# Kernel optimization log

Hardware: AMD Instinct MI355X
Metric: run time of the kernel (lower is better)

Reference implementation:

```python
import jax, jax.numpy as jnp
import numpy as np

N, D = 262144, 64
C, K, NSPLITS = 16, 4 + 12, 4  # K=16 codewords per codebook (2**NSPLITS)
K = 16
M = 16


def setup_inputs() -> dict:
    key = jax.random.key(0)
    k1, k2, k3, k4, k5 = jax.random.split(key, 5)
    A = jax.random.normal(k1, (N, D), dtype=jnp.float32)
    B = jax.random.normal(k2, (M, D), dtype=jnp.float32)
    prototypes = jax.random.normal(k3, (C, K, D), dtype=jnp.float32)
    split_dims = jax.random.randint(k4, (C, NSPLITS), 0, D, dtype=jnp.int32)
    # level i of the binary tree uses 2**i thresholds; pad to 2**(NSPLITS-1)=8
    split_vals = jax.random.normal(k5, (C, NSPLITS, 2 ** (NSPLITS - 1)), dtype=jnp.float32)
    return {"A": A, "B": B, "prototypes": prototypes,
            "split_dims": split_dims, "split_vals": split_vals}


def _encode(A, split_dims, split_vals):
    # Vectorized maddness_encode / apply_hash_function over all C codebooks.
    n = A.shape[0]
    c = split_dims.shape[0]
    nsplits = split_dims.shape[1]
    c_idx = jnp.arange(c)[None, :]                      # [1, C]
    group_ids = jnp.zeros((n, c), dtype=jnp.int32)      # [N, C]
    for i in range(nsplits):                            # fixed tiny loop (4 levels)
        x = A[:, split_dims[:, i]]                      # [N, C] gather of split dim
        vals_i = split_vals[:, i, :]                    # [C, 8]
        v = vals_i[c_idx, group_ids]                    # [N, C] per-group threshold
        group_ids = group_ids * 2 + (x > v).astype(jnp.int32)
    return group_ids                                    # [N, C] in [0, K)


def reference(A, B, prototypes, split_dims, split_vals):
    # 1) encode A rows: binary-tree hash per codebook -> codeword ids
    A_enc = _encode(A, split_dims, split_vals)          # [N, C] int32
    # 2) LUTs: luts[m, c, k] = <B[m], prototypes[c, k]>  (maddness_lut per row)
    luts = jnp.einsum('md,ckd->ckm', B, prototypes)     # [C, K, M]
    # 3) LUT-based accumulate (quantize_lut=False path): sum over codebooks
    c_idx = jnp.arange(luts.shape[0])[None, :]          # [1, C]
    g = luts[c_idx, A_enc]                              # [N, C, M] gathered LUT entries
    out = g.sum(axis=1).T                               # [M, N]
    return out
```

## Files before the change

### kernel.cpp

```cpp
#include <hip/hip_runtime.h>
#include <hip/hip_fp16.h>


#define NROWS 262144
#define DDIM  64
#define TPB   128
#define NBLK  2048
#define RSTR  129
#define LSTR  24

typedef __attribute__((ext_vector_type(8))) _Float16 half8;
typedef __attribute__((ext_vector_type(4))) unsigned int u32x4;

__global__ __launch_bounds__(256) void lut_build(
    const float* __restrict__ B,
    const float* __restrict__ P,
    _Float16* __restrict__ lutw)
{
    int o = blockIdx.x * 256 + threadIdx.x;
    int m  = o & 15;
    int ck = o >> 4;
    const float4* Bp = (const float4*)(B + m * DDIM);
    const float4* Pp = (const float4*)(P + ck * DDIM);
    float dot = 0.f;
    #pragma unroll
    for (int q = 0; q < 16; ++q) {
        float4 b = Bp[q], p = Pp[q];
        dot += b.x * p.x + b.y * p.y + b.z * p.z + b.w * p.w;
    }
    lutw[o] = (_Float16)dot;
}

__global__ __launch_bounds__(TPB, 2) void maddness_main(
    const float* __restrict__ A,
    const int*   __restrict__ sd,
    const float* __restrict__ sv,
    const _Float16* __restrict__ lutw,
    float* __restrict__ out)
{
    __shared__ float rows_s[DDIM * RSTR];
    __shared__ __align__(16) _Float16 lut_s[256 * LSTR];

    const int t = threadIdx.x;

    #pragma unroll
    for (int i = 0; i < 2; ++i) {
        int e = t + i * TPB;
        const u32x4* src = (const u32x4*)(lutw + e * 16);
        u32x4 q0 = src[0], q1 = src[1];
        *(u32x4*)(lut_s + e * LSTR)     = q0;
        *(u32x4*)(lut_s + e * LSTR + 8) = q1;
    }

    const float4* A4 = (const float4*)A;
    long base = (long)blockIdx.x * (TPB * DDIM / 4);
    float4 R[16];
    #pragma unroll
    for (int j = 0; j < 16; ++j) R[j] = A4[base + j * TPB + t];
    #pragma unroll
    for (int j = 0; j < 16; ++j) {
        int f    = j * TPB + t;
        int row  = f >> 4;
        int colq = (f & 15) * 4;
        rows_s[(colq + 0) * RSTR + row] = R[j].x;
        rows_s[(colq + 1) * RSTR + row] = R[j].y;
        rows_s[(colq + 2) * RSTR + row] = R[j].z;
        rows_s[(colq + 3) * RSTR + row] = R[j].w;
    }

    __syncthreads();

    half8 aE0 = {0,0,0,0,0,0,0,0}, aE1 = {0,0,0,0,0,0,0,0};
    half8 aO0 = {0,0,0,0,0,0,0,0}, aO1 = {0,0,0,0,0,0,0,0};

    #pragma unroll
    for (int c = 0; c < 16; ++c) {
        const int sd0 = sd[c*4+0], sd1 = sd[c*4+1], sd2 = sd[c*4+2], sd3 = sd[c*4+3];
        float x0 = rows_s[sd0 * RSTR + t];
        float x1 = rows_s[sd1 * RSTR + t];
        float x2 = rows_s[sd2 * RSTR + t];
        float x3 = rows_s[sd3 * RSTR + t];
        const float* svc = sv + c * 32;

        int g = (x0 > svc[0]) ? 1 : 0;
        float v1 = g ? svc[9] : svc[8];
        g = (g << 1) | ((x1 > v1) ? 1 : 0);
        float ta = (g & 1) ? svc[17] : svc[16];
        float tb = (g & 1) ? svc[19] : svc[18];
        float v2 = (g & 2) ? tb : ta;
        g = (g << 1) | ((x2 > v2) ? 1 : 0);
        float u0 = (g & 1) ? svc[25] : svc[24];
        float u1 = (g & 1) ? svc[27] : svc[26];
        float u2 = (g & 1) ? svc[29] : svc[28];
        float u3 = (g & 1) ? svc[31] : svc[30];
        float w0 = (g & 2) ? u1 : u0;
        float w1 = (g & 2) ? u3 : u2;
        float v3 = (g & 4) ? w1 : w0;
        g = (g << 1) | ((x3 > v3) ? 1 : 0);

        const _Float16* lp = lut_s + (c * 16 + g) * LSTR;
        half8 l0 = *(const half8*)(lp);
        half8 l1 = *(const half8*)(lp + 8);
        if (c & 1) { aO0 += l0; aO1 += l1; }
        else       { aE0 += l0; aE1 += l1; }
    }

    const int n = blockIdx.x * TPB + t;
    #pragma unroll
    for (int m = 0; m < 8; ++m) {
        out[(long)m       * NROWS + n] = (float)aE0[m] + (float)aO0[m];
        out[(long)(m + 8) * NROWS + n] = (float)aE1[m] + (float)aO1[m];
    }
}

extern "C" void kernel_launch(void* const* d_in, const int* in_sizes, int n_in,
                              void* d_out, int out_size, void* d_ws, size_t ws_size,
                              hipStream_t stream) {
    const float* A  = (const float*)d_in[0];
    const float* B  = (const float*)d_in[1];
    const float* P  = (const float*)d_in[2];
    const int*   sd = (const int*)d_in[3];
    const float* sv = (const float*)d_in[4];
    float* out = (float*)d_out;
    _Float16* lutw = (_Float16*)d_ws;

    lut_build<<<dim3(16), dim3(256), 0, stream>>>(B, P, lutw);
    maddness_main<<<dim3(NBLK), dim3(TPB), 0, stream>>>(A, sd, sv, lutw, out);
}
```

Baseline: 124.2 us.

## Use persistent 256-thread blocks with register-prefetched double tiles of A

Each block now has 256 threads and handles two 256-row tiles, launched as 512 blocks instead of 2048. While one tile is transposed into shared memory and hashed, the next tile's rows are prefetched into registers, and the LUT load into shared memory happens once per two tiles. This aims to overlap global loads with compute and amortize block setup. The launch bound still requests two blocks per CU at 256 threads, and larger shared memory per block may limit occupancy.

```diff
diff --git a/kernel.cpp b/kernel.cpp
--- a/kernel.cpp
+++ b/kernel.cpp
@@ -4,9 +4,11 @@
 
 #define NROWS 262144
 #define DDIM  64
-#define TPB   128
-#define NBLK  2048
-#define RSTR  129
+#define TPB   256
+#define ROWS  256
+#define TILES 2
+#define NBLK  512
+#define CSTR  261
 #define LSTR  24
 
 typedef __attribute__((ext_vector_type(8))) _Float16 half8;
@@ -38,78 +40,91 @@
     const _Float16* __restrict__ lutw,
     float* __restrict__ out)
 {
-    __shared__ float rows_s[DDIM * RSTR];
+    __shared__ float rows_s[DDIM * CSTR];
     __shared__ __align__(16) _Float16 lut_s[256 * LSTR];
 
     const int t = threadIdx.x;
 
-    #pragma unroll
-    for (int i = 0; i < 2; ++i) {
-        int e = t + i * TPB;
-        const u32x4* src = (const u32x4*)(lutw + e * 16);
+    {
+        const u32x4* src = (const u32x4*)(lutw + t * 16);
         u32x4 q0 = src[0], q1 = src[1];
-        *(u32x4*)(lut_s + e * LSTR)     = q0;
-        *(u32x4*)(lut_s + e * LSTR + 8) = q1;
+        *(u32x4*)(lut_s + t * LSTR)     = q0;
+        *(u32x4*)(lut_s + t * LSTR + 8) = q1;
     }
 
     const float4* A4 = (const float4*)A;
-    long base = (long)blockIdx.x * (TPB * DDIM / 4);
     float4 R[16];
-    #pragma unroll
-    for (int j = 0; j < 16; ++j) R[j] = A4[base + j * TPB + t];
-    #pragma unroll
-    for (int j = 0; j < 16; ++j) {
-        int f    = j * TPB + t;
-        int row  = f >> 4;
-        int colq = (f & 15) * 4;
-        rows_s[(colq + 0) * RSTR + row] = R[j].x;
-        rows_s[(colq + 1) * RSTR + row] = R[j].y;
-        rows_s[(colq + 2) * RSTR + row] = R[j].z;
-        rows_s[(colq + 3) * RSTR + row] = R[j].w;
+    {
+        long base = (long)blockIdx.x * (ROWS * DDIM / 4);
+        #pragma unroll
+        for (int j = 0; j < 16; ++j) R[j] = A4[base + j * TPB + t];
     }
 
-    __syncthreads();
+    for (int s = 0; s < TILES; ++s) {
+        const int tile = blockIdx.x + s * NBLK;
 
-    half8 aE0 = {0,0,0,0,0,0,0,0}, aE1 = {0,0,0,0,0,0,0,0};
-    half8 aO0 = {0,0,0,0,0,0,0,0}, aO1 = {0,0,0,0,0,0,0,0};
+        __syncthreads();
 
-    #pragma unroll
-    for (int c = 0; c < 16; ++c) {
-        const int sd0 = sd[c*4+0], sd1 = sd[c*4+1], sd2 = sd[c*4+2], sd3 = sd[c*4+3];
-        float x0 = rows_s[sd0 * RSTR + t];
-        float x1 = rows_s[sd1 * RSTR + t];
-        float x2 = rows_s[sd2 * RSTR + t];
-        float x3 = rows_s[sd3 * RSTR + t];
-        const float* svc = sv + c * 32;
+        #pragma unroll
+        for (int j = 0; j < 16; ++j) {
+            int f    = j * TPB + t;
+            int row  = f >> 4;
+            int colq = (f & 15) * 4;
+            rows_s[(colq + 0) * CSTR + row] = R[j].x;
+            rows_s[(colq + 1) * CSTR + row] = R[j].y;
+            rows_s[(colq + 2) * CSTR + row] = R[j].z;
+            rows_s[(colq + 3) * CSTR + row] = R[j].w;
+        }
+        if (s + 1 < TILES) {
+            long base = (long)(tile + NBLK) * (ROWS * DDIM / 4);
+            #pragma unroll
+            for (int j = 0; j < 16; ++j) R[j] = A4[base + j * TPB + t];
+        }
 
-        int g = (x0 > svc[0]) ? 1 : 0;
-        float v1 = g ? svc[9] : svc[8];
-        g = (g << 1) | ((x1 > v1) ? 1 : 0);
-        float ta = (g & 1) ? svc[17] : svc[16];
-        float tb = (g & 1) ? svc[19] : svc[18];
-        float v2 = (g & 2) ? tb : ta;
-        g = (g << 1) | ((x2 > v2) ? 1 : 0);
-        float u0 = (g & 1) ? svc[25] : svc[24];
-        float u1 = (g & 1) ? svc[27] : svc[26];
-        float u2 = (g & 1) ? svc[29] : svc[28];
-        float u3 = (g & 1) ? svc[31] : svc[30];
-        float w0 = (g & 2) ? u1 : u0;
-        float w1 = (g & 2) ? u3 : u2;
-        float v3 = (g & 4) ? w1 : w0;
-        g = (g << 1) | ((x3 > v3) ? 1 : 0);
+        __syncthreads();
 
-        const _Float16* lp = lut_s + (c * 16 + g) * LSTR;
-        half8 l0 = *(const half8*)(lp);
-        half8 l1 = *(const half8*)(lp + 8);
-        if (c & 1) { aO0 += l0; aO1 += l1; }
-        else       { aE0 += l0; aE1 += l1; }
-    }
+        half8 aE0 = {0,0,0,0,0,0,0,0}, aE1 = {0,0,0,0,0,0,0,0};
+        half8 aO0 = {0,0,0,0,0,0,0,0}, aO1 = {0,0,0,0,0,0,0,0};
 
-    const int n = blockIdx.x * TPB + t;
-    #pragma unroll
-    for (int m = 0; m < 8; ++m) {
-        out[(long)m       * NROWS + n] = (float)aE0[m] + (float)aO0[m];
-        out[(long)(m + 8) * NROWS + n] = (float)aE1[m] + (float)aO1[m];
+        #pragma unroll
+        for (int c = 0; c < 16; ++c) {
+            const int sd0 = sd[c*4+0], sd1 = sd[c*4+1];
+            const int sd2 = sd[c*4+2], sd3 = sd[c*4+3];
+            float x0 = rows_s[sd0 * CSTR + t];
+            float x1 = rows_s[sd1 * CSTR + t];
+            float x2 = rows_s[sd2 * CSTR + t];
+            float x3 = rows_s[sd3 * CSTR + t];
+            const float* svc = sv + c * 32;
+
+            int g = (x0 > svc[0]) ? 1 : 0;
+            float v1 = g ? svc[9] : svc[8];
+            g = (g << 1) | ((x1 > v1) ? 1 : 0);
+            float ta = (g & 1) ? svc[17] : svc[16];
+            float tb = (g & 1) ? svc[19] : svc[18];
+            float v2 = (g & 2) ? tb : ta;
+            g = (g << 1) | ((x2 > v2) ? 1 : 0);
+            float u0 = (g & 1) ? svc[25] : svc[24];
+            float u1 = (g & 1) ? svc[27] : svc[26];
+            float u2 = (g & 1) ? svc[29] : svc[28];
+            float u3 = (g & 1) ? svc[31] : svc[30];
+            float w0 = (g & 2) ? u1 : u0;
+            float w1 = (g & 2) ? u3 : u2;
+            float v3 = (g & 4) ? w1 : w0;
+            g = (g << 1) | ((x3 > v3) ? 1 : 0);
+
+            const _Float16* lp = lut_s + (c * 16 + g) * LSTR;
+            half8 l0 = *(const half8*)(lp);
+            half8 l1 = *(const half8*)(lp + 8);
+            if (c & 1) { aO0 += l0; aO1 += l1; }
+            else       { aE0 += l0; aE1 += l1; }
+        }
+
+        const int n = tile * ROWS + t;
+        #pragma unroll
+        for (int m = 0; m < 8; ++m) {
+            out[(long)m       * NROWS + n] = (float)aE0[m] + (float)aO0[m];
+            out[(long)(m + 8) * NROWS + n] = (float)aE1[m] + (float)aO1[m];
+        }
     }
 }
 
```

New measurement: 122.2 us. Within noise of the previous version (-1.6%).
